# Performance work log

Measured on AMD Instinct MI355X. Metric: run time of the kernel, lower is better.

Reference implementation:

```python
import jax, jax.numpy as jnp
import numpy as np

D_MODEL = 1024
NUM_HEADS = 16
D_HEAD = 64  # d_q = d_k = d_v
BATCH = 4
SEQ = 2048


def _trunc_normal(key, shape, std):
    # truncated normal in [-3*std, 3*std], matching nn.init.trunc_normal_
    return jax.random.truncated_normal(key, -3.0, 3.0, shape, dtype=jnp.float32) * std


def setup_inputs() -> dict:
    key = jax.random.key(0)
    k_x, k_q, k_k, k_v, k_o = jax.random.split(key, 5)
    hd = NUM_HEADS * D_HEAD
    s_in = np.sqrt(2.0 / (D_MODEL + hd))
    s_out = np.sqrt(2.0 / (hd + D_MODEL))
    return {
        "in_features": jax.random.normal(k_x, (BATCH, SEQ, D_MODEL), dtype=jnp.float32),
        "w_q": _trunc_normal(k_q, (hd, D_MODEL), s_in),
        "w_k": _trunc_normal(k_k, (hd, D_MODEL), s_in),
        "w_v": _trunc_normal(k_v, (hd, D_MODEL), s_in),
        "w_o": _trunc_normal(k_o, (D_MODEL, hd), s_out),
    }


def reference(in_features, w_q, w_k, w_v, w_o):
    B, S, D = in_features.shape
    H, Dh = NUM_HEADS, D_HEAD
    # QKV projections (weight stored as [out, in])
    q = jnp.einsum('od,bsd->bso', w_q, in_features).reshape(B, S, H, Dh).transpose(0, 2, 1, 3)
    k = jnp.einsum('od,bsd->bso', w_k, in_features).reshape(B, S, H, Dh).transpose(0, 2, 1, 3)
    v = jnp.einsum('od,bsd->bso', w_v, in_features).reshape(B, S, H, Dh).transpose(0, 2, 1, 3)
    # scaled dot-product attention with dense causal mask (as in source)
    att = jnp.einsum('bhqd,bhkd->bhqk', q, k) / jnp.sqrt(jnp.float32(Dh)).astype(q.dtype)
    causal = jnp.tril(jnp.ones((S, S), dtype=bool))
    att = jnp.where(causal, att, -jnp.inf)
    att = jax.nn.softmax(att, axis=-1)
    out = jnp.einsum('bhqk,bhkd->bhqd', att, v)  # [B,H,S,Dh]
    out = out.transpose(0, 2, 1, 3).reshape(B, S, H * Dh)
    return jnp.einsum('od,bsd->bso', w_o, out)
```

## Files before the change

kernel.cpp:

```cpp
#include <hip/hip_runtime.h>
#include <stdint.h>

#define D_MODEL 1024
#define NHEADS  16
#define DHEAD   64
#define BATCH   4
#define SEQ     2048
#define MTOT    (BATCH*SEQ)

typedef unsigned short u16;
typedef uint32_t u32;
typedef __bf16 bf16x8 __attribute__((ext_vector_type(8)));
typedef float  f32x4  __attribute__((ext_vector_type(4)));
typedef float  f32x16 __attribute__((ext_vector_type(16)));
typedef u16    u16x8  __attribute__((ext_vector_type(8)));
typedef u16    u16x4  __attribute__((ext_vector_type(4)));
typedef u32    u32x4  __attribute__((ext_vector_type(4)));

__device__ __forceinline__ u16 f2bf(float f) {
  uint32_t u = __builtin_bit_cast(uint32_t, f);
  u += 0x7fff + ((u >> 16) & 1);
  return (u16)(u >> 16);
}

__device__ __forceinline__ void gll16(const u16* g, u16* lds) {
  __builtin_amdgcn_global_load_lds(
      (__attribute__((address_space(1))) void*)(g),
      (__attribute__((address_space(3))) void*)(lds), 16, 0, 0);
}

__global__ void cvtk(const float4* __restrict__ in, u16x4* __restrict__ out, int n4) {
  const int i = blockIdx.x * blockDim.x + threadIdx.x;
  if (i < n4) {
    const float4 f = in[i];
    u16x4 h;
    h[0] = f2bf(f.x); h[1] = f2bf(f.y); h[2] = f2bf(f.z); h[3] = f2bf(f.w);
    out[i] = h;
  }
}

__global__ void cvtk4(const float4* __restrict__ a, const float4* __restrict__ b,
                      const float4* __restrict__ c, const float4* __restrict__ d,
                      u16x4* __restrict__ out, int n4) {
  const int i = blockIdx.x * blockDim.x + threadIdx.x;
  if (i >= n4) return;
  const float4* src = (blockIdx.y == 0) ? a : (blockIdx.y == 1) ? b
                    : (blockIdx.y == 2) ? c : d;
  const float4 f = src[i];
  u16x4 h;
  h[0] = f2bf(f.x); h[1] = f2bf(f.y); h[2] = f2bf(f.z); h[3] = f2bf(f.w);
  out[(size_t)blockIdx.y * n4 + i] = h;
}

#define QS 8192

#define BARS() __builtin_amdgcn_s_barrier()
#define LGKM0() do { asm volatile("s_waitcnt lgkmcnt(0)" ::: "memory"); \
                     __builtin_amdgcn_sched_barrier(0); } while (0)

#define STG(pbase, roff, t_, slot_) do {                                        \
    gll16((pbase) + (size_t)(roff)*1024 + (t_)*64,      qsm + (slot_)*QS + w*512);        \
    gll16((pbase) + (size_t)((roff)+64)*1024 + (t_)*64, qsm + (slot_)*QS + w*512 + 4096); \
  } while (0)

#define PH_READS_A() do {                                                       \
    _Pragma("unroll")                                                           \
    for (int mf = 0; mf < 8; ++mf) {                                            \
      af0[mf] = *(const bf16x8*)&sA[(mf*16 + r15)*64 + cs0];                    \
      af1[mf] = *(const bf16x8*)&sA[(mf*16 + r15)*64 + cs1];                    \
    }                                                                           \
    _Pragma("unroll")                                                           \
    for (int nf = 0; nf < 4; ++nf)                                              \
      bq[nf] = *(const bf16x8*)&sB[(brow + nf*16 + r15)*64 + cs0];              \
  } while (0)

#define PH_READS_B1() do {                                                      \
    _Pragma("unroll")                                                           \
    for (int nf = 0; nf < 4; ++nf)                                              \
      bq[nf] = *(const bf16x8*)&sB[(brow + nf*16 + r15)*64 + cs1];              \
  } while (0)

#define MM(AF, N0, N1) do {                                                     \
    __builtin_amdgcn_s_setprio(1);                                              \
    _Pragma("unroll")                                                           \
    for (int mf = 0; mf < 8; ++mf) {                                            \
      acc[mf][N0] = __builtin_amdgcn_mfma_f32_16x16x32_bf16(AF[mf], bq[N0],     \
                                                            acc[mf][N0], 0,0,0);\
      acc[mf][N1] = __builtin_amdgcn_mfma_f32_16x16x32_bf16(AF[mf], bq[N1],     \
                                                            acc[mf][N1], 0,0,0);\
    }                                                                           \
    __builtin_amdgcn_s_setprio(0);                                              \
  } while (0)

__global__ __launch_bounds__(512, 2) void gemm_qkv8p(
    const u16* __restrict__ A, const u16* __restrict__ Bw, u16* __restrict__ Out)
{
  extern __shared__ u16 qsm[];
  const int tid = threadIdx.x;
  const int w = tid >> 6, l = tid & 63;
  const int wm = w >> 2, wn = w & 3;
  const int bid = blockIdx.x;
  const int wg = (bid & 7) * 48 + (bid >> 3);
  const int m0 = (wg / 12) * 256, n0 = (wg % 12) * 256;

  const int sr  = 8*w + (l >> 3);
  const int sc8 = ((l & 7) ^ ((l >> 3) & 7)) * 8;
  const u16* pA = A  + (size_t)(m0 + sr) * 1024 + sc8;
  const u16* pB = Bw + (size_t)(n0 + sr) * 1024 + sc8;

  const int r15 = l & 15;
  const int cs0 = (((l >> 4) + 0) ^ (l & 7)) * 8;
  const int cs1 = (((l >> 4) + 4) ^ (l & 7)) * 8;
  const int brow = (wn & 1) * 64;

  f32x4 acc[8][4];
  #pragma unroll
  for (int i = 0; i < 8; ++i)
    #pragma unroll
    for (int j = 0; j < 4; ++j)
      acc[i][j] = f32x4{0.f, 0.f, 0.f, 0.f};

  STG(pA, 0,   0, 0);
  STG(pA, 128, 0, 1);
  STG(pB, 0,   0, 2);
  STG(pB, 128, 0, 3);
  STG(pA, 0,   1, 4);
  STG(pA, 128, 1, 5);
  STG(pB, 0,   1, 6);
  asm volatile("s_waitcnt vmcnt(6)" ::: "memory");
  BARS();
  __builtin_amdgcn_sched_barrier(0);

  #pragma unroll 2
  for (int t = 0; t < 14; ++t) {
    const int p = t & 1, po = p ^ 1;
    const u16* sA = qsm + (size_t)(p*4 + wm) * QS;
    const u16* sB = qsm + (size_t)(p*4 + 2 + (wn >> 1)) * QS;
    bf16x8 af0[8], af1[8], bq[4];
    PH_READS_A();
    STG(pB, 128, t+1, po*4 + 3);
    BARS(); LGKM0();
    MM(af0, 0, 1);
    BARS();
    STG(pA, 0, t+2, p*4 + 0);
    BARS();
    MM(af0, 2, 3);
    BARS();
    PH_READS_B1();
    STG(pA, 128, t+2, p*4 + 1);
    BARS(); LGKM0();
    MM(af1, 0, 1);
    BARS();
    STG(pB, 0, t+2, p*4 + 2);
    BARS();
    MM(af1, 2, 3);
    asm volatile("s_waitcnt vmcnt(6)" ::: "memory");
    BARS();
    __builtin_amdgcn_sched_barrier(0);
  }

  {
    const u16* sA = qsm + (size_t)(0*4 + wm) * QS;
    const u16* sB = qsm + (size_t)(0*4 + 2 + (wn >> 1)) * QS;
    bf16x8 af0[8], af1[8], bq[4];
    PH_READS_A();
    STG(pB, 128, 15, 4 + 3);
    BARS(); LGKM0();
    MM(af0, 0, 1);
    BARS();
    BARS();
    MM(af0, 2, 3);
    BARS();
    PH_READS_B1();
    BARS(); LGKM0();
    MM(af1, 0, 1);
    BARS();
    MM(af1, 2, 3);
    asm volatile("s_waitcnt vmcnt(0)" ::: "memory");
    BARS();
    __builtin_amdgcn_sched_barrier(0);
  }
  {
    const u16* sA = qsm + (size_t)(1*4 + wm) * QS;
    const u16* sB = qsm + (size_t)(1*4 + 2 + (wn >> 1)) * QS;
    bf16x8 af0[8], af1[8], bq[4];
    PH_READS_A();
    MM(af0, 0, 1);
    MM(af0, 2, 3);
    PH_READS_B1();
    MM(af1, 0, 1);
    MM(af1, 2, 3);
  }

  const float scale = (n0 < 1024) ? 0.125f * 1.44269504088896f : 1.0f;
  const int g = l >> 4, c15 = l & 15;
  #pragma unroll
  for (int mf = 0; mf < 8; ++mf) {
    #pragma unroll
    for (int nf = 0; nf < 4; ++nf) {
      #pragma unroll
      for (int j = 0; j < 4; ++j) {
        const int row = m0 + wm*128 + mf*16 + g*4 + j;
        const int col = n0 + wn*64 + nf*16 + c15;
        const int z = col >> 10;
        const int wi = col & 1023;
        const int b = row >> 11, sq = row & (SEQ-1);
        const int h = wi >> 6, dh = wi & (DHEAD-1);
        Out[(size_t)z * MTOT * D_MODEL
            + ((size_t)(b*NHEADS + h) * SEQ + sq) * DHEAD + dh] =
            f2bf(acc[mf][nf][j] * scale);
      }
    }
  }
}

#undef STG
#undef PH_READS_A
#undef PH_READS_B1
#undef MM

template<int MODE>
__launch_bounds__(256)
__global__ void gemm_bt_k(const u16* __restrict__ A,
                          const u16* __restrict__ W0,
                          const u16* __restrict__ W1,
                          const u16* __restrict__ W2,
                          void* __restrict__ Cout)
{
  constexpr int K = D_MODEL;
  const int tid = threadIdx.x;
  const int l = tid & 63, w = tid >> 6;
  const int m0 = blockIdx.x * 128;
  const int n0 = blockIdx.y * 128;
  const u16* Bm = W0;

  __shared__ __align__(16) u16 As[128*32];
  __shared__ __align__(16) u16 Bs[128*32];

  f32x4 acc[4][4];
  #pragma unroll
  for (int i = 0; i < 4; ++i)
    #pragma unroll
    for (int j = 0; j < 4; ++j)
      acc[i][j] = f32x4{0.f, 0.f, 0.f, 0.f};

  const int wr = w >> 1, wc = w & 1;
  const int srow = l >> 2;
  const int scol = (l & 3) * 8;

  for (int k0 = 0; k0 < K; k0 += 32) {
    __syncthreads();
    #pragma unroll
    for (int j = 0; j < 2; ++j) {
      const int seg = w * 2 + j;
      gll16(A  + (size_t)(m0 + seg*16 + srow) * K + k0 + scol, &As[seg*512]);
      gll16(Bm + (size_t)(n0 + seg*16 + srow) * K + k0 + scol, &Bs[seg*512]);
    }
    __syncthreads();
    bf16x8 af[4], bfr[4];
    #pragma unroll
    for (int m = 0; m < 4; ++m)
      af[m] = *(const bf16x8*)&As[(wr*64 + m*16 + (l & 15))*32 + (l >> 4)*8];
    #pragma unroll
    for (int n = 0; n < 4; ++n)
      bfr[n] = *(const bf16x8*)&Bs[(wc*64 + n*16 + (l & 15))*32 + (l >> 4)*8];
    #pragma unroll
    for (int m = 0; m < 4; ++m)
      #pragma unroll
      for (int n = 0; n < 4; ++n)
        acc[m][n] = __builtin_amdgcn_mfma_f32_16x16x32_bf16(af[m], bfr[n], acc[m][n], 0, 0, 0);
  }

  const int g = l >> 4, c15 = l & 15;
  #pragma unroll
  for (int m = 0; m < 4; ++m) {
    #pragma unroll
    for (int n = 0; n < 4; ++n) {
      #pragma unroll
      for (int j = 0; j < 4; ++j) {
        const int row = m0 + wr*64 + m*16 + g*4 + j;
        const int col = n0 + wc*64 + n*16 + c15;
        ((float*)Cout)[(size_t)row * D_MODEL + col] = acc[m][n][j];
      }
    }
  }
}

__launch_bounds__(512, 2)
__global__ void attn6_k(const u16* __restrict__ Qb, const u16* __restrict__ Kb_,
                        const u16* __restrict__ Vb_, u16* __restrict__ Oa)
{
  const int tid = threadIdx.x;
  const int w = tid >> 6, l = tid & 63;
  const int q5 = l & 31, hi = l >> 5;
  const int r = blockIdx.x;
  const int bh = (r & 7) * 8 + ((r >> 3) & 7);
  const int pairi = r >> 6;
  const int b = bh >> 4, h = bh & 15;
  const size_t base = (size_t)bh * SEQ * DHEAD;
  const u16* Qg = Qb + base;
  const u16* Kg = Kb_ + base;
  const u16* Vg = Vb_ + base;

  __shared__ __align__(16) u16 smem[32768];

  const int kc = tid & 7, rp = tid >> 3;
  const int vsub = rp >> 5;
  const int rp5 = rp & 31;
  int vIdx32[8];
  #pragma unroll
  for (int e = 0; e < 8; ++e)
    vIdx32[e] = vsub*2048 + (8*kc + e)*32 + ((((rp5 >> 2) ^ kc ^ e) & 7) << 2) + (rp5 & 3);

  const int kr8 = l >> 3;
  const int kkv = 8*w + kr8;
  const int kdc = (l & 7) ^ kr8 ^ w;

  for (int half = 0; half < 2; ++half) {
    const int tq = half ? (7 - pairi) : pairi;
    const int q0w = tq*256 + 32*w;
    const int ntk = (tq + 1) * 2;
    const int ntw = (q0w >> 7) + 1;

    bf16x8 qf[4];
    #pragma unroll
    for (int s = 0; s < 4; ++s)
      qf[s] = *(const bf16x8*)(Qg + (size_t)(q0w + q5)*DHEAD + 16*s + 8*hi);

    f32x16 c0 = {}, c1 = {};
    float mrun = -1e30f, lrun = 0.f;

    {
      #pragma unroll
      for (int h2 = 0; h2 < 2; ++h2)
        gll16(Kg + (size_t)(64*h2 + kkv)*DHEAD + kdc*8, smem + h2*4096 + w*512);
      const u16x8 v0 = *(const u16x8*)(Vg + (size_t)(2*rp)*DHEAD + kc*8);
      const u16x8 v1 = *(const u16x8*)(Vg + (size_t)(2*rp + 1)*DHEAD + kc*8);
      u32* Vd = (u32*)(smem + 16384);
      #pragma unroll
      for (int e = 0; e < 8; ++e)
        Vd[vIdx32[e]] = (u32)v0[e] | ((u32)v1[e] << 16);
    }
    __syncthreads();

    for (int t = 0; t < ntk; ++t) {
      const int cur = t & 1;
      const bool pf = (t + 1 < ntk);
      u16x8 v0, v1;
      if (pf) {
        const int kv1 = (t + 1) * 128;
        v0 = *(const u16x8*)(Vg + (size_t)(kv1 + 2*rp)*DHEAD + kc*8);
        v1 = *(const u16x8*)(Vg + (size_t)(kv1 + 2*rp + 1)*DHEAD + kc*8);
        #pragma unroll
        for (int h2 = 0; h2 < 2; ++h2)
          gll16(Kg + (size_t)(kv1 + 64*h2 + kkv)*DHEAD + kdc*8,
                smem + (cur^1)*8192 + h2*4096 + w*512);
      }

      if (t < ntw) {
        const u16* Kb = smem + cur*8192;
        const u16* Vv = smem + 16384 + cur*8192;

        f32x16 st[4] = {{}, {}, {}, {}};
        __builtin_amdgcn_s_setprio(1);
        #pragma unroll
        for (int kbg = 0; kbg < 4; ++kbg) {
          #pragma unroll
          for (int s = 0; s < 4; ++s) {
            const int slot = ((2*s + hi) ^ (l & 7) ^ ((4*(kbg & 1)) & 7) ^ (q5 >> 3)) & 7;
            const bf16x8 kf = *(const bf16x8*)(Kb + (kbg >> 1)*4096
                                               + ((kbg & 1)*32 + q5)*64 + slot*8);
            st[kbg] = __builtin_amdgcn_mfma_f32_32x32x16_bf16(kf, qf[s], st[kbg], 0, 0, 0);
          }
        }
        __builtin_amdgcn_s_setprio(0);

        if (t == ntw - 1) {
          const int kv0 = t * 128;
          #pragma unroll
          for (int kbg = 0; kbg < 4; ++kbg)
            #pragma unroll
            for (int rr = 0; rr < 16; ++rr) {
              const int kvg = kv0 + 32*kbg + (rr & 3) + 8*(rr >> 2) + 4*hi;
              if (kvg > q0w + q5) st[kbg][rr] = -1e30f;
            }
        }

        float mx = -1e30f;
        #pragma unroll
        for (int kbg = 0; kbg < 4; ++kbg)
          #pragma unroll
          for (int rr = 0; rr < 16; ++rr) mx = fmaxf(mx, st[kbg][rr]);
        mx = fmaxf(mx, __shfl_xor(mx, 32));
        float alpha = 1.0f;
        if (!__all(mx <= mrun + 8.0f)) {
          const float mnew = fmaxf(mrun, mx);
          alpha = __builtin_amdgcn_exp2f(mrun - mnew);
          mrun = mnew;
          #pragma unroll
          for (int rr = 0; rr < 16; ++rr) { c0[rr] *= alpha; c1[rr] *= alpha; }
        }
        float rs = 0.f;
        #pragma unroll
        for (int kbg = 0; kbg < 4; ++kbg)
          #pragma unroll
          for (int rr = 0; rr < 16; ++rr) {
            const float pe = __builtin_amdgcn_exp2f(st[kbg][rr] - mrun);
            st[kbg][rr] = pe;
            rs += pe;
          }
        rs += __shfl_xor(rs, 32);
        lrun = lrun * alpha + rs;

        bf16x8 pb[8];
        #pragma unroll
        for (int kbg = 0; kbg < 4; ++kbg) {
          u32 pw[8];
          #pragma unroll
          for (int i = 0; i < 8; ++i) {
            u32 t0;
            asm("v_cvt_pk_bf16_f32 %0, %1, %2"
                : "=v"(t0) : "v"(st[kbg][2*i]), "v"(st[kbg][2*i+1]));
            pw[i] = t0;
          }
          asm("v_permlane32_swap_b32 %0, %1" : "+v"(pw[0]), "+v"(pw[2]));
          asm("v_permlane32_swap_b32 %0, %1" : "+v"(pw[1]), "+v"(pw[3]));
          asm("v_permlane32_swap_b32 %0, %1" : "+v"(pw[4]), "+v"(pw[6]));
          asm("v_permlane32_swap_b32 %0, %1" : "+v"(pw[5]), "+v"(pw[7]));
          pb[2*kbg]   = __builtin_bit_cast(bf16x8, u32x4{pw[0], pw[1], pw[2], pw[3]});
          pb[2*kbg+1] = __builtin_bit_cast(bf16x8, u32x4{pw[4], pw[5], pw[6], pw[7]});
        }

        __builtin_amdgcn_s_setprio(1);
        #pragma unroll
        for (int h2 = 0; h2 < 2; ++h2) {
          #pragma unroll
          for (int s = 0; s < 4; ++s) {
            {
              const int slot = ((2*s + hi) ^ (l & 7) ^ (q5 >> 3)) & 7;
              const bf16x8 vf = *(const bf16x8*)(Vv + h2*4096 + q5*64 + slot*8);
              c0 = __builtin_amdgcn_mfma_f32_32x32x16_bf16(vf, pb[4*h2 + s], c0, 0, 0, 0);
            }
            {
              const int slot = ((2*s + hi) ^ (l & 7) ^ 4 ^ (q5 >> 3)) & 7;
              const bf16x8 vf = *(const bf16x8*)(Vv + h2*4096 + (32 + q5)*64 + slot*8);
              c1 = __builtin_amdgcn_mfma_f32_32x32x16_bf16(vf, pb[4*h2 + s], c1, 0, 0, 0);
            }
          }
        }
        __builtin_amdgcn_s_setprio(0);
      }

      if (pf) {
        u32* Vd = (u32*)(smem + 16384) + (cur^1)*4096;
        #pragma unroll
        for (int e = 0; e < 8; ++e)
          Vd[vIdx32[e]] = (u32)v0[e] | ((u32)v1[e] << 16);
      }
      __syncthreads();
    }

    const float linv = __builtin_amdgcn_rcpf(lrun);
    #pragma unroll
    for (int Ab = 0; Ab < 2; ++Ab)
      #pragma unroll
      for (int rr = 0; rr < 16; ++rr) {
        const int d = 32*Ab + (rr & 3) + 8*(rr >> 2) + 4*hi;
        smem[w*2048 + q5*64 + (((d >> 3) ^ (q5 & 7)) & 7)*8 + (d & 7)] =
            f2bf((Ab ? c1[rr] : c0[rr]) * linv);
      }
    __syncthreads();
    #pragma unroll
    for (int cc = 0; cc < 4; ++cc) {
      const int dchunk = 4*hi + cc;
      const u16x8 vv = *(const u16x8*)&smem[w*2048 + q5*64 + ((dchunk ^ (q5 & 7)) & 7)*8];
      *(u16x8*)(Oa + (size_t)(b*SEQ + q0w + q5)*D_MODEL + h*DHEAD + 32*hi + 8*cc) = vv;
    }
    __syncthreads();
  }
}

extern "C" void kernel_launch(void* const* d_in, const int* in_sizes, int n_in,
                              void* d_out, int out_size, void* d_ws, size_t ws_size,
                              hipStream_t stream) {
  const float* X  = (const float*)d_in[0];
  const float* Wq = (const float*)d_in[1];
  const float* Wk = (const float*)d_in[2];
  const float* Wv = (const float*)d_in[3];
  const float* Wo = (const float*)d_in[4];

  u16* xb  = (u16*)d_ws;
  u16* wqb = xb  + (size_t)MTOT*D_MODEL;
  u16* wkb = wqb + (size_t)D_MODEL*D_MODEL;
  u16* wvb = wkb + (size_t)D_MODEL*D_MODEL;
  u16* wob = wvb + (size_t)D_MODEL*D_MODEL;
  u16* qkv = wob + (size_t)D_MODEL*D_MODEL;
  u16* att = qkv + (size_t)3*MTOT*D_MODEL;

  (void)hipFuncSetAttribute((const void*)gemm_qkv8p,
                            hipFuncAttributeMaxDynamicSharedMemorySize, 131072);

  const int nx4 = MTOT*D_MODEL/4;
  const int nw4 = D_MODEL*D_MODEL/4;
  cvtk<<<nx4/256, 256, 0, stream>>>((const float4*)X, (u16x4*)xb, nx4);
  dim3 gc(nw4/256, 4, 1);
  cvtk4<<<gc, 256, 0, stream>>>((const float4*)Wq, (const float4*)Wk,
                                (const float4*)Wv, (const float4*)Wo,
                                (u16x4*)wqb, nw4);

  gemm_qkv8p<<<384, 512, 131072, stream>>>(xb, wqb, qkv);

  attn6_k<<<256, 512, 0, stream>>>(qkv, qkv + (size_t)MTOT*D_MODEL,
                                   qkv + (size_t)2*MTOT*D_MODEL, att);

  dim3 g3(MTOT/128, D_MODEL/128, 1);
  gemm_bt_k<0><<<g3, 256, 0, stream>>>(att, wob, nullptr, nullptr, d_out);
}
```

Before: 160.8 us.

## Replace output projection GEMM with pipelined 256x128 tile kernel using swizzled LDS

```diff
diff --git a/kernel.cpp b/kernel.cpp
--- a/kernel.cpp
+++ b/kernel.cpp
@@ -219,72 +219,143 @@
 #undef PH_READS_B1
 #undef MM
 
-template<int MODE>
-__launch_bounds__(256)
-__global__ void gemm_bt_k(const u16* __restrict__ A,
-                          const u16* __restrict__ W0,
-                          const u16* __restrict__ W1,
-                          const u16* __restrict__ W2,
-                          void* __restrict__ Cout)
+#define OSTG(pbase, roff, t_, slot_) do {                                       \
+    gll16((pbase) + (size_t)(roff)*1024 + (t_)*64,      osm + (slot_)*QS + w*512);        \
+    gll16((pbase) + (size_t)((roff)+64)*1024 + (t_)*64, osm + (slot_)*QS + w*512 + 4096); \
+  } while (0)
+
+#define OREADS_P1() do {                                                        \
+    _Pragma("unroll")                                                           \
+    for (int mf = 0; mf < 8; ++mf) {                                            \
+      af0[mf] = *(const bf16x8*)&sA[(mf*16 + r15)*64 + cs0];                    \
+      af1[mf] = *(const bf16x8*)&sA[(mf*16 + r15)*64 + cs1];                    \
+    }                                                                           \
+    _Pragma("unroll")                                                           \
+    for (int nf = 0; nf < 2; ++nf)                                              \
+      bq[nf] = *(const bf16x8*)&sB[(brow + nf*16 + r15)*64 + cs0];              \
+  } while (0)
+
+#define OREADS_P2() do {                                                        \
+    _Pragma("unroll")                                                           \
+    for (int nf = 0; nf < 2; ++nf)                                              \
+      bq[nf] = *(const bf16x8*)&sB[(brow + nf*16 + r15)*64 + cs1];              \
+  } while (0)
+
+#define OMM(AF) do {                                                            \
+    __builtin_amdgcn_s_setprio(1);                                              \
+    _Pragma("unroll")                                                           \
+    for (int mf = 0; mf < 8; ++mf) {                                            \
+      acc[mf][0] = __builtin_amdgcn_mfma_f32_16x16x32_bf16(AF[mf], bq[0],       \
+                                                           acc[mf][0], 0,0,0);  \
+      acc[mf][1] = __builtin_amdgcn_mfma_f32_16x16x32_bf16(AF[mf], bq[1],       \
+                                                           acc[mf][1], 0,0,0);  \
+    }                                                                           \
+    __builtin_amdgcn_s_setprio(0);                                              \
+  } while (0)
+
+__global__ __launch_bounds__(512, 2) void gemm_o8p(
+    const u16* __restrict__ A, const u16* __restrict__ Bw, float* __restrict__ Out)
 {
-  constexpr int K = D_MODEL;
+  extern __shared__ u16 osm[];
   const int tid = threadIdx.x;
-  const int l = tid & 63, w = tid >> 6;
-  const int m0 = blockIdx.x * 128;
-  const int n0 = blockIdx.y * 128;
-  const u16* Bm = W0;
-
-  __shared__ __align__(16) u16 As[128*32];
-  __shared__ __align__(16) u16 Bs[128*32];
-
-  f32x4 acc[4][4];
+  const int w = tid >> 6, l = tid & 63;
+  const int wm = w >> 2, wn = w & 3;
+  const int bid = blockIdx.x;
+  const int wg = (bid & 7) * 32 + (bid >> 3);
+  const int m0 = (wg >> 3) * 256, n0 = (wg & 7) * 128;
+
+  const int sr  = 8*w + (l >> 3);
+  const int sc8 = ((l & 7) ^ ((l >> 3) & 7)) * 8;
+  const u16* pA = A  + (size_t)(m0 + sr) * 1024 + sc8;
+  const u16* pB = Bw + (size_t)(n0 + sr) * 1024 + sc8;
+
+  const int r15 = l & 15;
+  const int cs0 = (((l >> 4) + 0) ^ (l & 7)) * 8;
+  const int cs1 = (((l >> 4) + 4) ^ (l & 7)) * 8;
+  const int brow = wn * 32;
+
+  f32x4 acc[8][2];
   #pragma unroll
-  for (int i = 0; i < 4; ++i)
-    #pragma unroll
-    for (int j = 0; j < 4; ++j)
-      acc[i][j] = f32x4{0.f, 0.f, 0.f, 0.f};
-
-  const int wr = w >> 1, wc = w & 1;
-  const int srow = l >> 2;
-  const int scol = (l & 3) * 8;
-
-  for (int k0 = 0; k0 < K; k0 += 32) {
-    __syncthreads();
-    #pragma unroll
-    for (int j = 0; j < 2; ++j) {
-      const int seg = w * 2 + j;
-      gll16(A  + (size_t)(m0 + seg*16 + srow) * K + k0 + scol, &As[seg*512]);
-      gll16(Bm + (size_t)(n0 + seg*16 + srow) * K + k0 + scol, &Bs[seg*512]);
-    }
-    __syncthreads();
-    bf16x8 af[4], bfr[4];
-    #pragma unroll
-    for (int m = 0; m < 4; ++m)
-      af[m] = *(const bf16x8*)&As[(wr*64 + m*16 + (l & 15))*32 + (l >> 4)*8];
-    #pragma unroll
-    for (int n = 0; n < 4; ++n)
-      bfr[n] = *(const bf16x8*)&Bs[(wc*64 + n*16 + (l & 15))*32 + (l >> 4)*8];
-    #pragma unroll
-    for (int m = 0; m < 4; ++m)
-      #pragma unroll
-      for (int n = 0; n < 4; ++n)
-        acc[m][n] = __builtin_amdgcn_mfma_f32_16x16x32_bf16(af[m], bfr[n], acc[m][n], 0, 0, 0);
+  for (int i = 0; i < 8; ++i) {
+    acc[i][0] = f32x4{0.f, 0.f, 0.f, 0.f};
+    acc[i][1] = f32x4{0.f, 0.f, 0.f, 0.f};
+  }
+
+  OSTG(pA, 0,   0, 0);
+  OSTG(pA, 128, 0, 1);
+  OSTG(pB, 0,   0, 2);
+  OSTG(pA, 0,   1, 3);
+  OSTG(pA, 128, 1, 4);
+  asm volatile("s_waitcnt vmcnt(4)" ::: "memory");
+  BARS();
+  __builtin_amdgcn_sched_barrier(0);
+
+  #pragma unroll 2
+  for (int t = 0; t < 14; ++t) {
+    const int p = t & 1, po = p ^ 1;
+    const u16* sA = osm + (size_t)(p*3 + wm) * QS;
+    const u16* sB = osm + (size_t)(p*3 + 2) * QS;
+    bf16x8 af0[8], af1[8], bq[2];
+    OREADS_P1();
+    OSTG(pB, 0, t+1, po*3 + 2);
+    BARS(); LGKM0();
+    OMM(af0);
+    BARS();
+    OREADS_P2();
+    OSTG(pA, 0,   t+2, p*3 + 0);
+    OSTG(pA, 128, t+2, p*3 + 1);
+    BARS(); LGKM0();
+    OMM(af1);
+    asm volatile("s_waitcnt vmcnt(4)" ::: "memory");
+    BARS();
+    __builtin_amdgcn_sched_barrier(0);
+  }
+
+  {
+    const u16* sA = osm + (size_t)(0*3 + wm) * QS;
+    const u16* sB = osm + (size_t)(0*3 + 2) * QS;
+    bf16x8 af0[8], af1[8], bq[2];
+    OREADS_P1();
+    OSTG(pB, 0, 15, 1*3 + 2);
+    BARS(); LGKM0();
+    OMM(af0);
+    BARS();
+    OREADS_P2();
+    BARS(); LGKM0();
+    OMM(af1);
+    asm volatile("s_waitcnt vmcnt(0)" ::: "memory");
+    BARS();
+    __builtin_amdgcn_sched_barrier(0);
+  }
+  {
+    const u16* sA = osm + (size_t)(1*3 + wm) * QS;
+    const u16* sB = osm + (size_t)(1*3 + 2) * QS;
+    bf16x8 af0[8], af1[8], bq[2];
+    OREADS_P1();
+    OMM(af0);
+    OREADS_P2();
+    OMM(af1);
   }
 
   const int g = l >> 4, c15 = l & 15;
   #pragma unroll
-  for (int m = 0; m < 4; ++m) {
+  for (int mf = 0; mf < 8; ++mf) {
     #pragma unroll
-    for (int n = 0; n < 4; ++n) {
+    for (int nf = 0; nf < 2; ++nf) {
       #pragma unroll
       for (int j = 0; j < 4; ++j) {
-        const int row = m0 + wr*64 + m*16 + g*4 + j;
-        const int col = n0 + wc*64 + n*16 + c15;
-        ((float*)Cout)[(size_t)row * D_MODEL + col] = acc[m][n][j];
+        const int row = m0 + wm*128 + mf*16 + g*4 + j;
+        const int col = n0 + wn*32 + nf*16 + c15;
+        Out[(size_t)row * D_MODEL + col] = acc[mf][nf][j];
       }
     }
   }
 }
+
+#undef OSTG
+#undef OREADS_P1
+#undef OREADS_P2
+#undef OMM
 
 __launch_bounds__(512, 2)
 __global__ void attn6_k(const u16* __restrict__ Qb, const u16* __restrict__ Kb_,
@@ -499,6 +570,8 @@
 
   (void)hipFuncSetAttribute((const void*)gemm_qkv8p,
                             hipFuncAttributeMaxDynamicSharedMemorySize, 131072);
+  (void)hipFuncSetAttribute((const void*)gemm_o8p,
+                            hipFuncAttributeMaxDynamicSharedMemorySize, 98304);
 
   const int nx4 = MTOT*D_MODEL/4;
   const int nw4 = D_MODEL*D_MODEL/4;
@@ -513,6 +586,5 @@
   attn6_k<<<256, 512, 0, stream>>>(qkv, qkv + (size_t)MTOT*D_MODEL,
                                    qkv + (size_t)2*MTOT*D_MODEL, att);
 
-  dim3 g3(MTOT/128, D_MODEL/128, 1);
-  gemm_bt_k<0><<<g3, 256, 0, stream>>>(att, wob, nullptr, nullptr, d_out);
-}
+  gemm_o8p<<<256, 512, 98304, stream>>>(att, wob, (float*)d_out);
+}
```

New measurement: 153.7 us. 1.05x faster.
